# Optimization experiments

Measured on AMD Instinct MI355X. Metric: run time of the kernel, lower is better.

The kernel has to match this reference:

```python
import jax, jax.numpy as jnp
import numpy as np

NUM_CLASSES = 1000
FEAT_DIM = 256
N = 262144
ALPHA = 0.5


def setup_inputs() -> dict:
    key = jax.random.key(0)
    k1, k2, k3 = jax.random.split(key, 3)
    features = jax.random.normal(k1, (N, FEAT_DIM), dtype=jnp.float32)
    labels = jax.random.randint(k2, (N,), 0, NUM_CLASSES, dtype=jnp.int64)
    centers = jax.random.normal(k3, (NUM_CLASSES, FEAT_DIM), dtype=jnp.float32)
    return {"features": features, "labels": labels, "centers": centers}


def reference(features, labels, centers):
    # Fused segment-mean: scatter-add of features + per-class counts,
    # replacing the per-class python loop in the original.
    sums = jax.ops.segment_sum(features, labels, num_segments=NUM_CLASSES)  # [C, D]
    counts = jax.ops.segment_sum(
        jnp.ones((features.shape[0],), dtype=features.dtype),
        labels,
        num_segments=NUM_CLASSES,
    )  # [C]
    has_samples = counts > 0
    safe_counts = jnp.where(has_samples, counts, 1.0)
    class_means = sums / safe_counts[:, None]  # [C, D]
    # EMA update only for classes present in the batch.
    updated = (1.0 - ALPHA) * centers + ALPHA * class_means
    new_centers = jnp.where(has_samples[:, None], updated, centers)
    return new_centers
```

## Files before the change

### kernel.cpp

```cpp
#include <hip/hip_runtime.h>

constexpr int N    = 262144;
constexpr int C    = 1000;
constexpr int D    = 256;
constexpr int D4   = 64;
constexpr int CPAD = 1024;
constexpr int NB   = 64;
constexpr int ROWS_PER_B = N / NB;
constexpr float ALPHA = 0.5f;

typedef float vfloat4 __attribute__((ext_vector_type(4)));


__global__ __launch_bounds__(256) void hist_kernel(
        const int* __restrict__ labels, int* __restrict__ hist,
        float4* __restrict__ sums4) {
    __shared__ int h[CPAD];
    int t = threadIdx.x;
    for (int i = t; i < CPAD; i += 256) h[i] = 0;
    for (int i = blockIdx.x * 256 + t; i < C * D / 4; i += NB * 256)
        sums4[i] = float4{0.f, 0.f, 0.f, 0.f};
    __syncthreads();
    int base = blockIdx.x * ROWS_PER_B;
    for (int i = t; i < ROWS_PER_B; i += 256)
        atomicAdd(&h[labels[base + i]], 1);
    __syncthreads();
    int* out = hist + blockIdx.x * CPAD;
    for (int i = t; i < CPAD; i += 256) out[i] = h[i];
}

__global__ __launch_bounds__(256) void scatter_kernel(
        const int* __restrict__ labels,
        const int* __restrict__ hist,
        int* __restrict__ counts,
        int* __restrict__ S) {
    __shared__ int s[CPAD];
    __shared__ int cu[CPAD];
    int t = threadIdx.x;
    int myb = blockIdx.x;

    int tot[4] = {0, 0, 0, 0};
    int pre[4] = {0, 0, 0, 0};
    for (int b = 0; b < NB; ++b) {
        #pragma unroll
        for (int c = 0; c < 4; ++c) {
            int v = hist[b * CPAD + c * 256 + t];
            tot[c] += v;
            if (b < myb) pre[c] += v;
        }
    }
    #pragma unroll
    for (int c = 0; c < 4; ++c) s[c * 256 + t] = tot[c];
    __syncthreads();
    for (int off = 1; off < CPAD; off <<= 1) {
        int add[4];
        #pragma unroll
        for (int c = 0; c < 4; ++c) {
            int idx = c * 256 + t;
            add[c] = (idx >= off) ? s[idx - off] : 0;
        }
        __syncthreads();
        #pragma unroll
        for (int c = 0; c < 4; ++c) s[c * 256 + t] += add[c];
        __syncthreads();
    }
    #pragma unroll
    for (int c = 0; c < 4; ++c) {
        int idx = c * 256 + t;
        cu[idx] = s[idx] - tot[c] + pre[c];
        if (myb == 0) counts[idx] = tot[c];
    }
    __syncthreads();

    int base = myb * ROWS_PER_B;
    for (int i = t; i < ROWS_PER_B; i += 256) {
        int row = base + i;
        int lab = labels[row];
        int pos = atomicAdd(&cu[lab], 1);
        S[pos] = (row << 10) | lab;
    }
}

__global__ __launch_bounds__(256) void seg_reduce_kernel(
        const vfloat4* __restrict__ feat4,
        const int* __restrict__ S,
        float* __restrict__ sums) {
    int wave = threadIdx.x >> 6;
    int lane = threadIdx.x & 63;
    int base = (blockIdx.x * 4 + wave) * 64;
    int packed = S[base + lane];

    vfloat4 acc = (vfloat4)0.f;
    int cur = __shfl(packed, 0) & 1023;

    #pragma unroll 1
    for (int i = 0; i < 64; i += 8) {
        int pk[8];
        vfloat4 v[8];
        #pragma unroll
        for (int j = 0; j < 8; ++j) pk[j] = __shfl(packed, i + j);
        #pragma unroll
        for (int j = 0; j < 8; ++j)
            v[j] = __builtin_nontemporal_load(&feat4[(long)(pk[j] >> 10) * D4 + lane]);
        #pragma unroll
        for (int j = 0; j < 8; ++j) {
            int lab = pk[j] & 1023;
            if (lab != cur) {
                float* dst = sums + cur * D + lane * 4;
                unsafeAtomicAdd(dst + 0, acc.x);
                unsafeAtomicAdd(dst + 1, acc.y);
                unsafeAtomicAdd(dst + 2, acc.z);
                unsafeAtomicAdd(dst + 3, acc.w);
                acc = (vfloat4)0.f;
                cur = lab;
            }
            acc += v[j];
        }
    }
    float* dst = sums + cur * D + lane * 4;
    unsafeAtomicAdd(dst + 0, acc.x);
    unsafeAtomicAdd(dst + 1, acc.y);
    unsafeAtomicAdd(dst + 2, acc.z);
    unsafeAtomicAdd(dst + 3, acc.w);
}

__global__ __launch_bounds__(256) void ema_kernel(
        const float4* __restrict__ cen4,
        const float* __restrict__ sums,
        const int* __restrict__ counts,
        float4* __restrict__ out4) {
    int idx = blockIdx.x * 256 + threadIdx.x;
    if (idx >= C * D4) return;
    int c = idx >> 6;
    int cnt = counts[c];
    float4 cen = cen4[idx];
    float4 o = cen;
    if (cnt > 0) {
        const float* sp = sums + c * D + (idx & 63) * 4;
        float s = ALPHA / (float)cnt;
        o.x = (1.0f - ALPHA) * cen.x + sp[0] * s;
        o.y = (1.0f - ALPHA) * cen.y + sp[1] * s;
        o.z = (1.0f - ALPHA) * cen.z + sp[2] * s;
        o.w = (1.0f - ALPHA) * cen.w + sp[3] * s;
    }
    out4[idx] = o;
}

extern "C" void kernel_launch(void* const* d_in, const int* in_sizes, int n_in,
                              void* d_out, int out_size, void* d_ws, size_t ws_size,
                              hipStream_t stream) {
    const vfloat4* feat4  = (const vfloat4*)d_in[0];
    const int*     labels = (const int*)d_in[1];
    const float4*  cen4   = (const float4*)d_in[2];
    float4*        out4   = (float4*)d_out;

    int*   hist   = (int*)d_ws;
    int*   counts = hist + NB * CPAD;
    int*   S      = counts + CPAD;
    float* sums   = (float*)(S + N);

    hist_kernel<<<NB, 256, 0, stream>>>(labels, hist, (float4*)sums);
    scatter_kernel<<<NB, 256, 0, stream>>>(labels, hist, counts, S);
    seg_reduce_kernel<<<N / 256, 256, 0, stream>>>(feat4, S, sums);
    ema_kernel<<<(C * D4 + 255) / 256, 256, 0, stream>>>(cen4, sums, counts, out4);
}
```

Before: 368.0 us.

## Replace counting-sort segment reduce with LDS-privatized per-slice partial sums

Drops the histogram/prefix-scan/scatter sort and the sorted segmented reduction with global atomics. Each block instead owns a 16-float feature slice and a row chunk, and accumulates per-class partial sums in a 64KB shared-memory table with a rotated bank layout. The EMA kernel then sums 32 chunk partials per element. This avoids the random row gathers and global atomics, at the cost of heavy LDS atomic contention, low occupancy from the large shared table, and extra partial-sum traffic.

```diff
diff --git a/kernel.cpp b/kernel.cpp
--- a/kernel.cpp
+++ b/kernel.cpp
@@ -1,147 +1,105 @@
 #include <hip/hip_runtime.h>
 
-constexpr int N    = 262144;
-constexpr int C    = 1000;
-constexpr int D    = 256;
-constexpr int D4   = 64;
-constexpr int CPAD = 1024;
-constexpr int NB   = 64;
-constexpr int ROWS_PER_B = N / NB;
+constexpr int N     = 262144;
+constexpr int C     = 1000;
+constexpr int D     = 256;
+constexpr int CPAD  = 1024;
+constexpr int NB    = 64;
+constexpr int SLICES = 16;
+constexpr int SDIM   = 16;
+constexpr int NCHUNK = 32;
+constexpr int ROWS_PER_CHUNK = N / NCHUNK;
+constexpr int TBL = C * SDIM;
 constexpr float ALPHA = 0.5f;
 
 typedef float vfloat4 __attribute__((ext_vector_type(4)));
 
 
 __global__ __launch_bounds__(256) void hist_kernel(
-        const int* __restrict__ labels, int* __restrict__ hist,
-        float4* __restrict__ sums4) {
+        const int* __restrict__ labels, int* __restrict__ counts) {
     __shared__ int h[CPAD];
     int t = threadIdx.x;
     for (int i = t; i < CPAD; i += 256) h[i] = 0;
-    for (int i = blockIdx.x * 256 + t; i < C * D / 4; i += NB * 256)
-        sums4[i] = float4{0.f, 0.f, 0.f, 0.f};
     __syncthreads();
-    int base = blockIdx.x * ROWS_PER_B;
-    for (int i = t; i < ROWS_PER_B; i += 256)
+    int base = blockIdx.x * (N / NB);
+    for (int i = t; i < N / NB; i += 256)
         atomicAdd(&h[labels[base + i]], 1);
     __syncthreads();
-    int* out = hist + blockIdx.x * CPAD;
-    for (int i = t; i < CPAD; i += 256) out[i] = h[i];
+    for (int i = t; i < CPAD; i += 256)
+        if (h[i]) atomicAdd(&counts[i], h[i]);
 }
 
-__global__ __launch_bounds__(256) void scatter_kernel(
+__global__ __launch_bounds__(256) void partial_kernel(
+        const vfloat4* __restrict__ feat4,
         const int* __restrict__ labels,
-        const int* __restrict__ hist,
-        int* __restrict__ counts,
-        int* __restrict__ S) {
-    __shared__ int s[CPAD];
-    __shared__ int cu[CPAD];
+        float* __restrict__ partials) {
+    __shared__ float tbl[TBL];
     int t = threadIdx.x;
-    int myb = blockIdx.x;
+    for (int i = t; i < TBL; i += 256) tbl[i] = 0.f;
+    __syncthreads();
 
-    int tot[4] = {0, 0, 0, 0};
-    int pre[4] = {0, 0, 0, 0};
-    for (int b = 0; b < NB; ++b) {
+    int s     = blockIdx.x >> 5;
+    int chunk = blockIdx.x & 31;
+    int q     = t & 3;
+    int rg    = t >> 2;
+    int base  = chunk * ROWS_PER_CHUNK;
+
+    #pragma unroll 1
+    for (int outer = 0; outer < ROWS_PER_CHUNK / 64; outer += 8) {
+        int lab[8];
+        vfloat4 v[8];
         #pragma unroll
-        for (int c = 0; c < 4; ++c) {
-            int v = hist[b * CPAD + c * 256 + t];
-            tot[c] += v;
-            if (b < myb) pre[c] += v;
+        for (int j = 0; j < 8; ++j) {
+            int row = base + (outer + j) * 64 + rg;
+            lab[j] = labels[row];
+            v[j]   = feat4[(long)row * 64 + s * 4 + q];
         }
-    }
-    #pragma unroll
-    for (int c = 0; c < 4; ++c) s[c * 256 + t] = tot[c];
-    __syncthreads();
-    for (int off = 1; off < CPAD; off <<= 1) {
-        int add[4];
         #pragma unroll
-        for (int c = 0; c < 4; ++c) {
-            int idx = c * 256 + t;
-            add[c] = (idx >= off) ? s[idx - off] : 0;
+        for (int j = 0; j < 8; ++j) {
+            int cl = lab[j];
+            int b0 = q * 4 + cl;
+            atomicAdd(&tbl[cl * SDIM + ((b0 + 0) & 15)], v[j].x);
+            atomicAdd(&tbl[cl * SDIM + ((b0 + 1) & 15)], v[j].y);
+            atomicAdd(&tbl[cl * SDIM + ((b0 + 2) & 15)], v[j].z);
+            atomicAdd(&tbl[cl * SDIM + ((b0 + 3) & 15)], v[j].w);
         }
-        __syncthreads();
-        #pragma unroll
-        for (int c = 0; c < 4; ++c) s[c * 256 + t] += add[c];
-        __syncthreads();
-    }
-    #pragma unroll
-    for (int c = 0; c < 4; ++c) {
-        int idx = c * 256 + t;
-        cu[idx] = s[idx] - tot[c] + pre[c];
-        if (myb == 0) counts[idx] = tot[c];
     }
     __syncthreads();
 
-    int base = myb * ROWS_PER_B;
-    for (int i = t; i < ROWS_PER_B; i += 256) {
-        int row = base + i;
-        int lab = labels[row];
-        int pos = atomicAdd(&cu[lab], 1);
-        S[pos] = (row << 10) | lab;
+    float* dst = partials + (long)blockIdx.x * TBL;
+    for (int i = t; i < TBL; i += 256) {
+        int cl = i >> 4, d = i & 15;
+        dst[i] = tbl[cl * SDIM + ((d + cl) & 15)];
     }
-}
-
-__global__ __launch_bounds__(256) void seg_reduce_kernel(
-        const vfloat4* __restrict__ feat4,
-        const int* __restrict__ S,
-        float* __restrict__ sums) {
-    int wave = threadIdx.x >> 6;
-    int lane = threadIdx.x & 63;
-    int base = (blockIdx.x * 4 + wave) * 64;
-    int packed = S[base + lane];
-
-    vfloat4 acc = (vfloat4)0.f;
-    int cur = __shfl(packed, 0) & 1023;
-
-    #pragma unroll 1
-    for (int i = 0; i < 64; i += 8) {
-        int pk[8];
-        vfloat4 v[8];
-        #pragma unroll
-        for (int j = 0; j < 8; ++j) pk[j] = __shfl(packed, i + j);
-        #pragma unroll
-        for (int j = 0; j < 8; ++j)
-            v[j] = __builtin_nontemporal_load(&feat4[(long)(pk[j] >> 10) * D4 + lane]);
-        #pragma unroll
-        for (int j = 0; j < 8; ++j) {
-            int lab = pk[j] & 1023;
-            if (lab != cur) {
-                float* dst = sums + cur * D + lane * 4;
-                unsafeAtomicAdd(dst + 0, acc.x);
-                unsafeAtomicAdd(dst + 1, acc.y);
-                unsafeAtomicAdd(dst + 2, acc.z);
-                unsafeAtomicAdd(dst + 3, acc.w);
-                acc = (vfloat4)0.f;
-                cur = lab;
-            }
-            acc += v[j];
-        }
-    }
-    float* dst = sums + cur * D + lane * 4;
-    unsafeAtomicAdd(dst + 0, acc.x);
-    unsafeAtomicAdd(dst + 1, acc.y);
-    unsafeAtomicAdd(dst + 2, acc.z);
-    unsafeAtomicAdd(dst + 3, acc.w);
 }
 
 __global__ __launch_bounds__(256) void ema_kernel(
         const float4* __restrict__ cen4,
-        const float* __restrict__ sums,
+        const float* __restrict__ partials,
         const int* __restrict__ counts,
         float4* __restrict__ out4) {
     int idx = blockIdx.x * 256 + threadIdx.x;
-    if (idx >= C * D4) return;
-    int c = idx >> 6;
+    if (idx >= C * 64) return;
+    int c   = idx >> 6;
+    int d4  = idx & 63;
+    int s   = d4 >> 2;
+    int dis = (d4 & 3) * 4;
     int cnt = counts[c];
     float4 cen = cen4[idx];
     float4 o = cen;
     if (cnt > 0) {
-        const float* sp = sums + c * D + (idx & 63) * 4;
-        float s = ALPHA / (float)cnt;
-        o.x = (1.0f - ALPHA) * cen.x + sp[0] * s;
-        o.y = (1.0f - ALPHA) * cen.y + sp[1] * s;
-        o.z = (1.0f - ALPHA) * cen.z + sp[2] * s;
-        o.w = (1.0f - ALPHA) * cen.w + sp[3] * s;
+        float sx = 0.f, sy = 0.f, sz = 0.f, sw = 0.f;
+        const float* p = partials + (long)s * NCHUNK * TBL + c * SDIM + dis;
+        #pragma unroll 8
+        for (int ch = 0; ch < NCHUNK; ++ch) {
+            const float* pp = p + (long)ch * TBL;
+            sx += pp[0]; sy += pp[1]; sz += pp[2]; sw += pp[3];
+        }
+        float sc = ALPHA / (float)cnt;
+        o.x = (1.0f - ALPHA) * cen.x + sx * sc;
+        o.y = (1.0f - ALPHA) * cen.y + sy * sc;
+        o.z = (1.0f - ALPHA) * cen.z + sz * sc;
+        o.w = (1.0f - ALPHA) * cen.w + sw * sc;
     }
     out4[idx] = o;
 }
@@ -154,13 +112,11 @@
     const float4*  cen4   = (const float4*)d_in[2];
     float4*        out4   = (float4*)d_out;
 
-    int*   hist   = (int*)d_ws;
-    int*   counts = hist + NB * CPAD;
-    int*   S      = counts + CPAD;
-    float* sums   = (float*)(S + N);
+    int*   counts   = (int*)d_ws;
+    float* partials = (float*)(counts + CPAD);
 
-    hist_kernel<<<NB, 256, 0, stream>>>(labels, hist, (float4*)sums);
-    scatter_kernel<<<NB, 256, 0, stream>>>(labels, hist, counts, S);
-    seg_reduce_kernel<<<N / 256, 256, 0, stream>>>(feat4, S, sums);
-    ema_kernel<<<(C * D4 + 255) / 256, 256, 0, stream>>>(cen4, sums, counts, out4);
+    hipMemsetAsync(counts, 0, CPAD * sizeof(int), stream);
+    hist_kernel<<<NB, 256, 0, stream>>>(labels, counts);
+    partial_kernel<<<SLICES * NCHUNK, 256, 0, stream>>>(feat4, labels, partials);
+    ema_kernel<<<(C * 64 + 255) / 256, 256, 0, stream>>>(cen4, partials, counts, out4);
 }
```

New measurement: 617.4 us. 1.68x slower.
